# Performance work log

Hardware: AMD Instinct MI355X
Metric: run time of the kernel (lower is better)

Reference implementation:

```python
import jax, jax.numpy as jnp
import numpy as np

N = 100000   # nodes
E = 1250000  # directed edges
K = 20000    # selected nodes
D_IN, D_H, D_OUT = 128, 64, 5
NEG_SLOPE = 0.01  # F.leaky_relu default
EPS = 1e-5        # BatchNorm eps


def setup_inputs() -> dict:
    key = jax.random.key(0)
    ks = jax.random.split(key, 13)
    x = jax.random.normal(ks[0], (N, D_IN), jnp.float32)
    edge_index = jax.random.randint(ks[1], (2, E), 0, N, dtype=jnp.int32)
    idx = jax.random.randint(ks[2], (K,), 0, N, dtype=jnp.int32)
    # GCNConv 0: glorot-style weights + zero bias
    W0 = jax.random.normal(ks[3], (D_IN, D_H), jnp.float32) * (1.0 / np.sqrt(D_IN))
    b0 = jnp.zeros((D_H,), jnp.float32)
    gamma0 = jnp.ones((D_H,), jnp.float32)
    beta0 = jnp.zeros((D_H,), jnp.float32)
    # GCNConv 1
    W1 = jax.random.normal(ks[4], (D_H, D_H), jnp.float32) * (1.0 / np.sqrt(D_H))
    b1 = jnp.zeros((D_H,), jnp.float32)
    gamma1 = jnp.ones((D_H,), jnp.float32)
    beta1 = jnp.zeros((D_H,), jnp.float32)
    # final MLP
    Wm = jax.random.normal(ks[5], (D_H, D_OUT), jnp.float32) * (1.0 / np.sqrt(D_H))
    bm = jnp.zeros((D_OUT,), jnp.float32)
    return {"x": x, "edge_index": edge_index, "idx": idx,
            "W0": W0, "b0": b0, "gamma0": gamma0, "beta0": beta0,
            "W1": W1, "b1": b1, "gamma1": gamma1, "beta1": beta1,
            "Wm": Wm, "bm": bm}


def reference(x, edge_index, idx, W0, b0, gamma0, beta0, W1, b1, gamma1, beta1, Wm, bm):
    n = x.shape[0]
    # GCNConv: add self-loops, symmetric normalization D^-1/2 A D^-1/2
    loops = jnp.arange(n, dtype=edge_index.dtype)
    row = jnp.concatenate([edge_index[0], loops])  # source
    col = jnp.concatenate([edge_index[1], loops])  # target
    deg = jax.ops.segment_sum(jnp.ones_like(col, dtype=x.dtype), col, num_segments=n)
    dis = jnp.where(deg > 0, jax.lax.rsqrt(jnp.maximum(deg, 1e-12)), 0.0)
    norm = dis[row] * dis[col]  # [E+N]

    def gcn_conv(h, W, b):
        hw = h @ W                                  # [N, d_out]
        msg = hw[row] * norm[:, None]               # gather + scale
        return jax.ops.segment_sum(msg, col, num_segments=n) + b  # scatter-add

    def batch_norm(h, g, b):  # training-mode BN over node dim
        mu = h.mean(axis=0)
        var = h.var(axis=0)
        return (h - mu) * jax.lax.rsqrt(var + EPS) * g + b

    h = jax.nn.leaky_relu(gcn_conv(x, W0, b0), NEG_SLOPE)
    h = batch_norm(h, gamma0, beta0)
    h = jax.nn.leaky_relu(gcn_conv(h, W1, b1), NEG_SLOPE)
    h = batch_norm(h, gamma1, beta1)
    h_sel = h[idx]                                   # index_select over nodes
    out = jax.nn.sigmoid(h_sel @ Wm + bm)
    return (h_sel, out)
```

## Files before the change

kernel.cpp:

```cpp
#include <hip/hip_runtime.h>

static constexpr float NEG_SLOPE = 0.01f;
static constexpr float BN_EPS = 1e-5f;

using f16 = _Float16;
using f16x4 = __attribute__((ext_vector_type(4))) _Float16;
using f32x4 = __attribute__((ext_vector_type(4))) float;

__global__ __launch_bounds__(256) void sentinel_kernel(float* out, int m, float val) {
  int i = blockIdx.x * 256 + threadIdx.x;
  if (i < m) out[i] = val;
}

__global__ __launch_bounds__(256) void zero_kernel(int* __restrict__ deg,
                                                   float* __restrict__ stats,
                                                   int* __restrict__ csr_pad, int n) {
  int stride = gridDim.x * blockDim.x;
  for (int i = blockIdx.x * blockDim.x + threadIdx.x; i < n; i += stride) deg[i] = 0;
  if (blockIdx.x == 0 && threadIdx.x < 256) stats[threadIdx.x] = 0.f;
  if (blockIdx.x == 0 && threadIdx.x < 16) csr_pad[threadIdx.x] = 0;
}

__global__ __launch_bounds__(256) void deg_kernel(const int* __restrict__ col,
                                                  int* __restrict__ deg, int E) {
  int stride = gridDim.x * blockDim.x;
  for (int i = blockIdx.x * blockDim.x + threadIdx.x; i < E; i += stride)
    atomicAdd(&deg[col[i]], 1);
}

__global__ __launch_bounds__(256) void scan_partial(const int* __restrict__ deg,
                                                    int* __restrict__ partial, int n) {
  int i = blockIdx.x * 256 + threadIdx.x;
  int v = (i < n) ? deg[i] : 0;
  __shared__ int s[256];
  s[threadIdx.x] = v;
  __syncthreads();
  for (int off = 128; off; off >>= 1) {
    if (threadIdx.x < off) s[threadIdx.x] += s[threadIdx.x + off];
    __syncthreads();
  }
  if (threadIdx.x == 0) partial[blockIdx.x] = s[0];
}

__global__ __launch_bounds__(256) void scan_top(int* partial, int nb) {
  __shared__ int s[256];
  __shared__ int carry_s;
  if (threadIdx.x == 0) carry_s = 0;
  __syncthreads();
  for (int base = 0; base < nb; base += 256) {
    int i = base + threadIdx.x;
    int v = (i < nb) ? partial[i] : 0;
    s[threadIdx.x] = v;
    __syncthreads();
    for (int off = 1; off < 256; off <<= 1) {
      int t = (threadIdx.x >= off) ? s[threadIdx.x - off] : 0;
      __syncthreads();
      s[threadIdx.x] += t;
      __syncthreads();
    }
    int inc = s[threadIdx.x];
    int tot = s[255];
    int carry = carry_s;
    if (i < nb) partial[i] = carry + inc - v;
    __syncthreads();
    if (threadIdx.x == 0) carry_s = carry + tot;
    __syncthreads();
  }
}

__global__ __launch_bounds__(256) void scan_final(const int* __restrict__ deg,
                                                  const int* __restrict__ partial,
                                                  int* __restrict__ start,
                                                  float* __restrict__ dis, int n, int E) {
  int i = blockIdx.x * 256 + threadIdx.x;
  int v = (i < n) ? deg[i] : 0;
  __shared__ int s[256];
  s[threadIdx.x] = v;
  __syncthreads();
  for (int off = 1; off < 256; off <<= 1) {
    int t = (threadIdx.x >= off) ? s[threadIdx.x - off] : 0;
    __syncthreads();
    s[threadIdx.x] += t;
    __syncthreads();
  }
  if (i < n) {
    start[i] = partial[blockIdx.x] + s[threadIdx.x] - v;
    dis[i] = rsqrtf((float)(v + 1));
  }
  if (i == 0) start[n] = E;
}

__global__ __launch_bounds__(256) void fill_kernel(
    const int* __restrict__ row, const int* __restrict__ colv,
    const int* __restrict__ start, int* __restrict__ deg,
    int* __restrict__ csr, int E) {
  int stride = gridDim.x * blockDim.x;
  for (int e = blockIdx.x * blockDim.x + threadIdx.x; e < E; e += stride) {
    int v = colv[e];
    int o = atomicSub(&deg[v], 1) - 1;
    csr[start[v] + o] = row[e];
  }
}

template <int KD, bool FOLD, bool A_HALF>
__global__ __launch_bounds__(256) void mfma_gemm(
    const void* __restrict__ Aptr, const float* __restrict__ W,
    const float* __restrict__ sc, const float* __restrict__ cadd,
    const float* __restrict__ dis, f16* __restrict__ g, int n) {
  constexpr int NKT = KD / 16;
  const int lane = threadIdx.x & 63;
  const int wq = threadIdx.x >> 6;
  const int lr = lane & 15;
  const int kb = (lane >> 4) * 4;

  f16x4 bfrag[NKT][4];
#pragma unroll
  for (int kt = 0; kt < NKT; ++kt)
#pragma unroll
    for (int ct = 0; ct < 4; ++ct) {
#pragma unroll
      for (int j = 0; j < 4; ++j) {
        int k = kt * 16 + kb + j;
        float w = W[k * 64 + ct * 16 + lr];
        if (FOLD) w *= sc[k];
        bfrag[kt][ct][j] = (f16)w;
      }
    }
  float cl[4];
#pragma unroll
  for (int ct = 0; ct < 4; ++ct) cl[ct] = FOLD ? cadd[ct * 16 + lr] : 0.f;

  const int ntiles = (n + 15) >> 4;
  for (int t = blockIdx.x * 4 + wq; t < ntiles; t += gridDim.x * 4) {
    const int r0 = t << 4;
    int arow = r0 + lr;
    if (arow >= n) arow = n - 1;
    f16x4 afrag[NKT];
    if (A_HALF) {
      const f16* Ah = (const f16*)Aptr;
#pragma unroll
      for (int kt = 0; kt < NKT; ++kt)
        afrag[kt] = *reinterpret_cast<const f16x4*>(Ah + (size_t)arow * KD + kt * 16 + kb);
    } else {
      const float* Af = (const float*)Aptr;
#pragma unroll
      for (int kt = 0; kt < NKT; ++kt) {
        f32x4 xa = *reinterpret_cast<const f32x4*>(Af + (size_t)arow * KD + kt * 16 + kb);
        f16x4 a;
        a[0] = (f16)xa[0]; a[1] = (f16)xa[1]; a[2] = (f16)xa[2]; a[3] = (f16)xa[3];
        afrag[kt] = a;
      }
    }
    f32x4 acc[4];
#pragma unroll
    for (int ct = 0; ct < 4; ++ct) acc[ct] = (f32x4){0.f, 0.f, 0.f, 0.f};
#pragma unroll
    for (int kt = 0; kt < NKT; ++kt)
#pragma unroll
      for (int ct = 0; ct < 4; ++ct)
        acc[ct] = __builtin_amdgcn_mfma_f32_16x16x16f16(afrag[kt], bfrag[kt][ct], acc[ct], 0, 0, 0);
    if (r0 + 16 <= n) {
#pragma unroll
      for (int v = 0; v < 4; ++v) {
        int grow = r0 + (lane >> 4) * 4 + v;
        float dv = dis[grow];
#pragma unroll
        for (int ct = 0; ct < 4; ++ct)
          g[(size_t)grow * 64 + ct * 16 + lr] = (f16)((acc[ct][v] + cl[ct]) * dv);
      }
    } else {
      for (int v = 0; v < 4; ++v) {
        int grow = r0 + (lane >> 4) * 4 + v;
        if (grow < n) {
          float dv = dis[grow];
          for (int ct = 0; ct < 4; ++ct)
            g[(size_t)grow * 64 + ct * 16 + lr] = (f16)((acc[ct][v] + cl[ct]) * dv);
        }
      }
    }
  }
}

template <typename OutT>
__global__ __launch_bounds__(256) void gather_post(
    const f16* __restrict__ g, const int* __restrict__ csr,
    const int* __restrict__ start, const float* __restrict__ dis,
    const float* __restrict__ bias, OutT* __restrict__ t_out,
    float* __restrict__ stats, int n) {
  const int lane = threadIdx.x & 63;
  const float bd = bias[lane];
  const int wid = (blockIdx.x * 256 + threadIdx.x) >> 6;
  const int nw = (gridDim.x * 256) >> 6;
  float lsum = 0.f, lsq = 0.f;
  for (int v = wid; v < n; v += nw) {
    int s0 = start[v];
    int s1 = start[v + 1];
    float sum = (float)g[(size_t)v * 64 + lane];
    for (int e = s0; e < s1; e += 16) {
      int u[16];
#pragma unroll
      for (int i = 0; i < 16; ++i) u[i] = (e + i < s1) ? csr[e + i] : v;
      float a[16];
#pragma unroll
      for (int i = 0; i < 16; ++i) a[i] = (float)g[(size_t)u[i] * 64 + lane];
      float part = 0.f;
#pragma unroll
      for (int i = 0; i < 16; ++i) part += (e + i < s1) ? a[i] : 0.f;
      sum += part;
    }
    float t = dis[v] * sum + bd;
    t = (t > 0.f) ? t : NEG_SLOPE * t;
    t_out[(size_t)v * 64 + lane] = (OutT)t;
    lsum += t;
    lsq += t * t;
  }
  __shared__ float red[256];
  red[threadIdx.x] = lsum;
  __syncthreads();
  if (threadIdx.x < 64)
    atomicAdd(&stats[lane],
              red[threadIdx.x] + red[threadIdx.x + 64] + red[threadIdx.x + 128] + red[threadIdx.x + 192]);
  __syncthreads();
  red[threadIdx.x] = lsq;
  __syncthreads();
  if (threadIdx.x < 64)
    atomicAdd(&stats[64 + lane],
              red[threadIdx.x] + red[threadIdx.x + 64] + red[threadIdx.x + 128] + red[threadIdx.x + 192]);
}

__global__ __launch_bounds__(64) void bnparam_kernel(
    const float* __restrict__ stats, const float* __restrict__ gamma,
    const float* __restrict__ beta, const float* __restrict__ W,
    float* __restrict__ outp, int n, int withC) {
  int d = threadIdx.x;
  __shared__ float ssh[64];
  float inv_n = 1.0f / (float)n;
  float mu = stats[d] * inv_n;
  float var = stats[64 + d] * inv_n - mu * mu;
  float r = rsqrtf(var + BN_EPS);
  float s = gamma[d] * r;
  float sh = beta[d] - mu * s;
  outp[d] = s;
  outp[64 + d] = sh;
  ssh[d] = sh;
  __syncthreads();
  if (withC) {
    float c = 0.f;
    for (int k = 0; k < 64; ++k) c = fmaf(ssh[k], W[k * 64 + d], c);
    outp[128 + d] = c;
  }
}

__global__ __launch_bounds__(256) void selmlp_kernel(
    const float* __restrict__ t, const int* __restrict__ idx,
    const float* __restrict__ bnp, const float* __restrict__ Wm,
    const float* __restrict__ bm, float* __restrict__ out,
    float* __restrict__ out2, int K) {
  const int lane = threadIdx.x & 63;
  int w = (blockIdx.x * 256 + threadIdx.x) >> 6;
  if (w >= K) return;
  int v = idx[w];
  float hv = fmaf(t[(size_t)v * 64 + lane], bnp[lane], bnp[64 + lane]);
  out[(size_t)w * 64 + lane] = hv;
#pragma unroll
  for (int j = 0; j < 5; ++j) {
    float p = hv * Wm[lane * 5 + j];
#pragma unroll
    for (int off = 32; off; off >>= 1) p += __shfl_xor(p, off);
    if (lane == 0) out2[(size_t)w * 5 + j] = 1.f / (1.f + expf(-(p + bm[j])));
  }
}

extern "C" void kernel_launch(void* const* d_in, const int* in_sizes, int n_in,
                              void* d_out, int out_size, void* d_ws, size_t ws_size,
                              hipStream_t stream) {
  const float* x      = (const float*)d_in[0];
  const int*   eidx   = (const int*)d_in[1];
  const int*   idx    = (const int*)d_in[2];
  const float* W0     = (const float*)d_in[3];
  const float* b0     = (const float*)d_in[4];
  const float* gamma0 = (const float*)d_in[5];
  const float* beta0  = (const float*)d_in[6];
  const float* W1     = (const float*)d_in[7];
  const float* b1     = (const float*)d_in[8];
  const float* gamma1 = (const float*)d_in[9];
  const float* beta1  = (const float*)d_in[10];
  const float* Wm     = (const float*)d_in[11];
  const float* bm     = (const float*)d_in[12];

  const int n = in_sizes[0] / 128;
  const int E = in_sizes[1] / 2;
  const int K = in_sizes[2];
  const int* erow = eidx;
  const int* ecol = eidx + E;
  const int nb = (n + 255) / 256;

  size_t needed = (size_t)n * 64 * 4
                + 256 * 4 + 320 * 4
                + (size_t)n * 4
                + (size_t)n * 4
                + (size_t)(n + 1) * 4
                + (size_t)(E + 16) * 4
                + (size_t)(nb + 1) * 4
                + (size_t)n * 64 * 2
                + (size_t)n * 64 * 2;
  if (ws_size < needed) {
    sentinel_kernel<<<dim3((out_size + 255) / 256), dim3(256), 0, stream>>>(
        (float*)d_out, out_size, 1e6f);
    return;
  }
  float* tf    = (float*)d_ws;
  float* stats = tf + (size_t)n * 64;
  float* bnp   = stats + 256;
  float* dis   = bnp + 320;
  int*   deg   = (int*)(dis + n);
  int*   start = deg + n;
  int*   csr   = start + (n + 1);
  int*   partial = csr + (E + 16);
  f16*   gh    = (f16*)(partial + nb + 1);
  f16*   t0h   = gh + (size_t)n * 64;

  dim3 blk(256);
  zero_kernel<<<dim3(nb), blk, 0, stream>>>(deg, stats, csr + E, n);
  deg_kernel<<<dim3(2048), blk, 0, stream>>>(ecol, deg, E);
  scan_partial<<<dim3(nb), blk, 0, stream>>>(deg, partial, n);
  scan_top<<<dim3(1), blk, 0, stream>>>(partial, nb);
  scan_final<<<dim3(nb), blk, 0, stream>>>(deg, partial, start, dis, n, E);
  fill_kernel<<<dim3(2048), blk, 0, stream>>>(erow, ecol, start, deg, csr, E);

  mfma_gemm<128, false, false><<<dim3(640), blk, 0, stream>>>(
      x, W0, nullptr, nullptr, dis, gh, n);
  gather_post<f16><<<dim3(2048), blk, 0, stream>>>(gh, csr, start, dis, b0, t0h, stats, n);
  bnparam_kernel<<<dim3(1), dim3(64), 0, stream>>>(stats, gamma0, beta0, W1, bnp, n, 1);
  mfma_gemm<64, true, true><<<dim3(640), blk, 0, stream>>>(
      t0h, W1, bnp, bnp + 128, dis, gh, n);
  gather_post<float><<<dim3(2048), blk, 0, stream>>>(gh, csr, start, dis, b1, tf, stats + 128, n);
  bnparam_kernel<<<dim3(1), dim3(64), 0, stream>>>(
      stats + 128, gamma1, beta1, nullptr, bnp + 192, n, 0);
  selmlp_kernel<<<dim3((K + 3) / 4), blk, 0, stream>>>(
      tf, idx, bnp + 192, Wm, bm, (float*)d_out, (float*)d_out + (size_t)K * 64, K);
}
```

Before: 361.3 us.

## Batch atomics in CSR build and process two nodes per wave in gather

The degree and fill kernels now handle four edges per thread, issuing all loads before the atomics so memory requests overlap. A separate cursor array holding inclusive prefix sums lets fill write directly to the returned slot, dropping the extra start[] lookup. The gather kernel now has each wavefront aggregate two consecutive nodes together, issuing both neighbor gathers at once to raise memory-level parallelism. The cost is higher register pressure and wasted padded loads when the two nodes' degrees differ.

```diff
diff --git a/kernel.cpp b/kernel.cpp
--- a/kernel.cpp
+++ b/kernel.cpp
@@ -13,19 +13,25 @@
 }
 
 __global__ __launch_bounds__(256) void zero_kernel(int* __restrict__ deg,
-                                                   float* __restrict__ stats,
-                                                   int* __restrict__ csr_pad, int n) {
+                                                   float* __restrict__ stats, int n) {
   int stride = gridDim.x * blockDim.x;
   for (int i = blockIdx.x * blockDim.x + threadIdx.x; i < n; i += stride) deg[i] = 0;
   if (blockIdx.x == 0 && threadIdx.x < 256) stats[threadIdx.x] = 0.f;
-  if (blockIdx.x == 0 && threadIdx.x < 16) csr_pad[threadIdx.x] = 0;
 }
 
 __global__ __launch_bounds__(256) void deg_kernel(const int* __restrict__ col,
                                                   int* __restrict__ deg, int E) {
-  int stride = gridDim.x * blockDim.x;
-  for (int i = blockIdx.x * blockDim.x + threadIdx.x; i < E; i += stride)
-    atomicAdd(&deg[col[i]], 1);
+  int t = blockIdx.x * 256 + threadIdx.x;
+  int S = gridDim.x * 256;
+  int e0 = t, e1 = t + S, e2 = t + 2 * S, e3 = t + 3 * S;
+  int v0 = (e0 < E) ? col[e0] : -1;
+  int v1 = (e1 < E) ? col[e1] : -1;
+  int v2 = (e2 < E) ? col[e2] : -1;
+  int v3 = (e3 < E) ? col[e3] : -1;
+  if (v0 >= 0) atomicAdd(&deg[v0], 1);
+  if (v1 >= 0) atomicAdd(&deg[v1], 1);
+  if (v2 >= 0) atomicAdd(&deg[v2], 1);
+  if (v3 >= 0) atomicAdd(&deg[v3], 1);
 }
 
 __global__ __launch_bounds__(256) void scan_partial(const int* __restrict__ deg,
@@ -71,6 +77,7 @@
 __global__ __launch_bounds__(256) void scan_final(const int* __restrict__ deg,
                                                   const int* __restrict__ partial,
                                                   int* __restrict__ start,
+                                                  int* __restrict__ cursor,
                                                   float* __restrict__ dis, int n, int E) {
   int i = blockIdx.x * 256 + threadIdx.x;
   int v = (i < n) ? deg[i] : 0;
@@ -84,7 +91,9 @@
     __syncthreads();
   }
   if (i < n) {
-    start[i] = partial[blockIdx.x] + s[threadIdx.x] - v;
+    int incl = partial[blockIdx.x] + s[threadIdx.x];
+    start[i] = incl - v;
+    cursor[i] = incl;
     dis[i] = rsqrtf((float)(v + 1));
   }
   if (i == 0) start[n] = E;
@@ -92,14 +101,25 @@
 
 __global__ __launch_bounds__(256) void fill_kernel(
     const int* __restrict__ row, const int* __restrict__ colv,
-    const int* __restrict__ start, int* __restrict__ deg,
-    int* __restrict__ csr, int E) {
-  int stride = gridDim.x * blockDim.x;
-  for (int e = blockIdx.x * blockDim.x + threadIdx.x; e < E; e += stride) {
-    int v = colv[e];
-    int o = atomicSub(&deg[v], 1) - 1;
-    csr[start[v] + o] = row[e];
-  }
+    int* __restrict__ cursor, int* __restrict__ csr, int E) {
+  int t = blockIdx.x * 256 + threadIdx.x;
+  int S = gridDim.x * 256;
+  int e0 = t, e1 = t + S, e2 = t + 2 * S, e3 = t + 3 * S;
+  bool b0 = e0 < E, b1 = e1 < E, b2 = e2 < E, b3 = e3 < E;
+  int v0 = 0, v1 = 0, v2 = 0, v3 = 0, r0 = 0, r1 = 0, r2 = 0, r3 = 0;
+  if (b0) { v0 = colv[e0]; r0 = row[e0]; }
+  if (b1) { v1 = colv[e1]; r1 = row[e1]; }
+  if (b2) { v2 = colv[e2]; r2 = row[e2]; }
+  if (b3) { v3 = colv[e3]; r3 = row[e3]; }
+  int o0 = 0, o1 = 0, o2 = 0, o3 = 0;
+  if (b0) o0 = atomicSub(&cursor[v0], 1) - 1;
+  if (b1) o1 = atomicSub(&cursor[v1], 1) - 1;
+  if (b2) o2 = atomicSub(&cursor[v2], 1) - 1;
+  if (b3) o3 = atomicSub(&cursor[v3], 1) - 1;
+  if (b0) csr[o0] = r0;
+  if (b1) csr[o1] = r1;
+  if (b2) csr[o2] = r2;
+  if (b3) csr[o3] = r3;
 }
 
 template <int KD, bool FOLD, bool A_HALF>
@@ -189,30 +209,56 @@
     float* __restrict__ stats, int n) {
   const int lane = threadIdx.x & 63;
   const float bd = bias[lane];
+  const f16* gl = g + lane;
   const int wid = (blockIdx.x * 256 + threadIdx.x) >> 6;
   const int nw = (gridDim.x * 256) >> 6;
   float lsum = 0.f, lsq = 0.f;
-  for (int v = wid; v < n; v += nw) {
-    int s0 = start[v];
-    int s1 = start[v + 1];
-    float sum = (float)g[(size_t)v * 64 + lane];
-    for (int e = s0; e < s1; e += 16) {
-      int u[16];
-#pragma unroll
-      for (int i = 0; i < 16; ++i) u[i] = (e + i < s1) ? csr[e + i] : v;
-      float a[16];
-#pragma unroll
-      for (int i = 0; i < 16; ++i) a[i] = (float)g[(size_t)u[i] * 64 + lane];
-      float part = 0.f;
-#pragma unroll
-      for (int i = 0; i < 16; ++i) part += (e + i < s1) ? a[i] : 0.f;
-      sum += part;
-    }
-    float t = dis[v] * sum + bd;
-    t = (t > 0.f) ? t : NEG_SLOPE * t;
-    t_out[(size_t)v * 64 + lane] = (OutT)t;
-    lsum += t;
-    lsq += t * t;
+  for (int v0 = wid * 2; v0 < n; v0 += nw * 2) {
+    const int v1 = v0 + 1;
+    const bool hasB = (v1 < n);
+    int2 sv = *reinterpret_cast<const int2*>(start + v0);
+    const int s0a = sv.x, s1a = sv.y;
+    const int s0b = s1a;
+    const int s1b = hasB ? start[v0 + 2] : s1a;
+    float suma = (float)gl[v0 * 64];
+    float sumb = hasB ? (float)gl[v1 * 64] : 0.f;
+    int ea = s0a, eb = s0b;
+    int nbat_a = (s1a - s0a + 15) >> 4;
+    int nbat_b = (s1b - s0b + 15) >> 4;
+    int nbatch = nbat_a > nbat_b ? nbat_a : nbat_b;
+    for (int b = 0; b < nbatch; ++b) {
+      int ua[16], ub[16];
+#pragma unroll
+      for (int i = 0; i < 16; ++i) ua[i] = (ea + i < s1a) ? csr[ea + i] : v0;
+#pragma unroll
+      for (int i = 0; i < 16; ++i) ub[i] = (eb + i < s1b) ? csr[eb + i] : v0;
+      float fa[16], fb[16];
+#pragma unroll
+      for (int i = 0; i < 16; ++i) fa[i] = (float)gl[ua[i] * 64];
+#pragma unroll
+      for (int i = 0; i < 16; ++i) fb[i] = (float)gl[ub[i] * 64];
+      float pa = 0.f, pb = 0.f;
+#pragma unroll
+      for (int i = 0; i < 16; ++i) pa += (ea + i < s1a) ? fa[i] : 0.f;
+#pragma unroll
+      for (int i = 0; i < 16; ++i) pb += (eb + i < s1b) ? fb[i] : 0.f;
+      suma += pa;
+      sumb += pb;
+      ea += 16;
+      eb += 16;
+    }
+    float ta = dis[v0] * suma + bd;
+    ta = (ta > 0.f) ? ta : NEG_SLOPE * ta;
+    t_out[(size_t)v0 * 64 + lane] = (OutT)ta;
+    lsum += ta;
+    lsq += ta * ta;
+    if (hasB) {
+      float tb = dis[v1] * sumb + bd;
+      tb = (tb > 0.f) ? tb : NEG_SLOPE * tb;
+      t_out[(size_t)v1 * 64 + lane] = (OutT)tb;
+      lsum += tb;
+      lsq += tb * tb;
+    }
   }
   __shared__ float red[256];
   red[threadIdx.x] = lsum;
@@ -300,6 +346,7 @@
                 + (size_t)n * 4
                 + (size_t)n * 4
                 + (size_t)(n + 1) * 4
+                + (size_t)n * 4
                 + (size_t)(E + 16) * 4
                 + (size_t)(nb + 1) * 4
                 + (size_t)n * 64 * 2
@@ -315,18 +362,20 @@
   float* dis   = bnp + 320;
   int*   deg   = (int*)(dis + n);
   int*   start = deg + n;
-  int*   csr   = start + (n + 1);
+  int*   cursor = start + (n + 1);
+  int*   csr   = cursor + n;
   int*   partial = csr + (E + 16);
   f16*   gh    = (f16*)(partial + nb + 1);
   f16*   t0h   = gh + (size_t)n * 64;
 
   dim3 blk(256);
-  zero_kernel<<<dim3(nb), blk, 0, stream>>>(deg, stats, csr + E, n);
-  deg_kernel<<<dim3(2048), blk, 0, stream>>>(ecol, deg, E);
+  const int eb4 = (E + 1023) / 1024;
+  zero_kernel<<<dim3(nb), blk, 0, stream>>>(deg, stats, n);
+  deg_kernel<<<dim3(eb4), blk, 0, stream>>>(ecol, deg, E);
   scan_partial<<<dim3(nb), blk, 0, stream>>>(deg, partial, n);
   scan_top<<<dim3(1), blk, 0, stream>>>(partial, nb);
-  scan_final<<<dim3(nb), blk, 0, stream>>>(deg, partial, start, dis, n, E);
-  fill_kernel<<<dim3(2048), blk, 0, stream>>>(erow, ecol, start, deg, csr, E);
+  scan_final<<<dim3(nb), blk, 0, stream>>>(deg, partial, start, cursor, dis, n, E);
+  fill_kernel<<<dim3(eb4), blk, 0, stream>>>(erow, ecol, cursor, csr, E);
 
   mfma_gemm<128, false, false><<<dim3(640), blk, 0, stream>>>(
       x, W0, nullptr, nullptr, dis, gh, n);
```

After: 371.3 us. +2.8%, slower.
